# Kernel optimization log

Hardware: AMD Instinct MI355X
Metric: run time of the kernel (lower is better)

Reference implementation:

```python
import jax, jax.numpy as jnp
import numpy as np

BOARD = 19
MAX_DIST = 18
# 4 line directions then 4 diagonal directions (LINE_GROUP=[0,1,2,3], DIAG_GROUP=[4,5,6,7])
DIRS = [(-1, 0), (1, 0), (0, -1), (0, 1), (-1, -1), (-1, 1), (1, -1), (1, 1)]


def build_ray_buffer(max_dist=MAX_DIST, n=BOARD):
    """flat_index [8, max_dist, n*n] int32, valid_mask [8, max_dist, n*n] float32."""
    hs, ws = np.meshgrid(np.arange(n), np.arange(n), indexing='ij')  # [n,n]
    hs = hs.reshape(-1)
    ws = ws.reshape(-1)
    r = np.arange(1, max_dist + 1)[:, None]  # [max_dist,1]
    idx = np.zeros((8, max_dist, n * n), np.int32)
    mask = np.zeros((8, max_dist, n * n), np.float32)
    for d, (dh, dw) in enumerate(DIRS):
        hh = hs[None, :] + dh * r  # [max_dist, n*n]
        ww = ws[None, :] + dw * r
        ok = (hh >= 0) & (hh < n) & (ww >= 0) & (ww < n)
        idx[d] = np.where(ok, hh * n + ww, 0).astype(np.int32)
        mask[d] = ok.astype(np.float32)
    return jnp.asarray(idx), jnp.asarray(mask)


def setup_inputs() -> dict:
    key = jax.random.key(0)
    k_x, k_w = jax.random.split(key)
    B, c_in, c_out, md = 128, 32, 64, MAX_DIST
    x = jax.random.normal(k_x, (B, c_in, BOARD, BOARD), dtype=jnp.float32)
    # init: normal(0, sqrt(2/fan_in)) scaled by distance decay (decay=1.0)
    fan_in = c_in * 2 * md
    scale = (2.0 / fan_in) ** 0.5
    weight = scale * jax.random.normal(k_w, (c_out, c_in, 2, md), dtype=jnp.float32)
    decay = 1.0 / jnp.arange(1, md + 1, dtype=jnp.float32)
    weight = weight.at[:, :, 0, :].multiply(decay)
    weight = weight.at[:, :, 1, :].multiply(decay * 0.7)
    bias = jnp.zeros((c_out,), dtype=jnp.float32)
    flat_index, valid_mask = build_ray_buffer()
    return {"x": x, "weight": weight, "bias": bias,
            "flat_index": flat_index, "valid_mask": valid_mask}


def reference(x, weight, bias, flat_index, valid_mask):
    B, C, H, W = x.shape
    c_out = weight.shape[0]
    md = weight.shape[-1]
    # D8 symmetry expansion: lines (dirs 0-3) share weight[...,0,:], diagonals (4-7) share weight[...,1,:]
    w_full = jnp.concatenate([
        jnp.broadcast_to(weight[:, :, 0:1, :], (c_out, C, 4, md)),
        jnp.broadcast_to(weight[:, :, 1:2, :], (c_out, C, 4, md)),
    ], axis=2)  # [c_out, C, 8, md]
    x_flat = x.reshape(B, C, H * W)
    # gather along rays: [B, C, 8, md, H*W]
    gathered = x_flat[:, :, flat_index] * valid_mask  # mask broadcasts [8, md, HW]
    gathered = gathered.reshape(B, C, 8, md, H, W)
    # NOTE: faithful to original torch einsum 'bcdrhw,ocdR->bohw' — 'r' and 'R'
    # are DISTINCT labels, so distance is independently summed on each operand.
    out = jnp.einsum('bcdrhw,ocdR->bohw', gathered, w_full)
    return out + bias[None, :, None, None]
```

## Files before the change

### kernel.cpp

```cpp
#include <hip/hip_runtime.h>

#define C_IN 32
#define C_OUT 64
#define NB 128
#define HW 361
#define SXS 364
#define SSS 132
#define WS 36

__global__ __launch_bounds__(256) void prep_w_kernel(const float* __restrict__ weight,
                                                     float* __restrict__ wsf) {
  int t = blockIdx.x * blockDim.x + threadIdx.x;
  if (t >= C_OUT * C_IN) return;
  int o = t >> 5;
  int c = t & 31;
  const float* wp = weight + (size_t)((o * C_IN + c) * 2) * 18;
  float sl = 0.f, sd = 0.f;
#pragma unroll
  for (int r = 0; r < 18; ++r) { sl += wp[r]; sd += wp[18 + r]; }
  wsf[c * 64 + o] = sl;
  wsf[2048 + c * 64 + o] = sd;
  wsf[4096 + c * 64 + o] = -2.f * (sl + sd);
}

__global__ __launch_bounds__(256) void raycast_main_kernel(
    const float* __restrict__ x, const float* __restrict__ bias,
    const float* __restrict__ wsf, float* __restrict__ out) {
  __shared__ __align__(16) float sm[23584];
  float* const sx    = sm;
  float* const ssum  = sm + 11648;
  float* const pproj = sm + 15872;
  float* const swl   = sm + 20096;
  float* const swd   = sm + 21248;
  float* const swld2 = sm + 22400;
  float* const sbias = sm + 23552;

  const int tid = threadIdx.x;
  const int b = blockIdx.x >> 1;
  const int obase = (blockIdx.x & 1) << 5;

  for (int i = tid; i < 3 * 1024; i += 256) {
    int arr = i >> 10;
    int rem = i & 1023;
    int c = rem >> 5;
    int j = rem & 31;
    sm[20096 + arr * 1152 + c * WS + j] = wsf[arr * 2048 + c * 64 + obase + j];
  }
  if (tid < 32) sbias[tid] = bias[obase + tid];

  const float4* x4 = reinterpret_cast<const float4*>(x + (size_t)b * (C_IN * HW));
  for (int i = tid; i < (C_IN * HW) / 4; i += 256) {
    float4 v = x4[i];
    float vv[4] = {v.x, v.y, v.z, v.w};
    int e = i * 4;
#pragma unroll
    for (int j = 0; j < 4; ++j) {
      int ee = e + j;
      int c = ee / HW;
      int hw = ee - c * HW;
      sx[c * SXS + hw] = vv[j];
    }
  }
  __syncthreads();

  for (int t = tid; t < 608; t += 256) {
    int c = t / 19, h = t - c * 19;
    const float* p = sx + c * SXS + h * 19;
    float s = 0.f;
#pragma unroll
    for (int w = 0; w < 19; ++w) s += p[w];
    ssum[c * SSS + h] = s;
  }
  for (int t = tid; t < 608; t += 256) {
    int c = t / 19, w = t - c * 19;
    const float* p = sx + c * SXS + w;
    float s = 0.f;
#pragma unroll
    for (int h = 0; h < 19; ++h) s += p[h * 19];
    ssum[c * SSS + 20 + w] = s;
  }
  for (int t = tid; t < 1184; t += 256) {
    int c = t / 37, k = t - c * 37;
    int hmin = k > 18 ? k - 18 : 0;
    int hmax = k < 18 ? k : 18;
    const float* p = sx + c * SXS + (18 - k);
    float s = 0.f;
    for (int h = hmin; h <= hmax; ++h) s += p[h * 20];
    ssum[c * SSS + 40 + k] = s;
  }
  for (int t = tid; t < 1184; t += 256) {
    int c = t / 37, k = t - c * 37;
    int hmin = k > 18 ? k - 18 : 0;
    int hmax = k < 18 ? k : 18;
    const float* p = sx + c * SXS + k;
    float s = 0.f;
    for (int h = hmin; h <= hmax; ++h) s += p[h * 18];
    ssum[c * SSS + 80 + k] = s;
  }
  __syncthreads();

  if (tid < 240) {
    int ot = tid / 30, st = tid - ot * 30;
    int o0 = ot * 4, s0 = st * 4;
    const float* wT = (s0 < 40) ? swl : swd;
    float a[4][4] = {};
#pragma unroll 4
    for (int c = 0; c < 32; ++c) {
      float4 wv = *reinterpret_cast<const float4*>(wT + c * WS + o0);
      float4 sv = *reinterpret_cast<const float4*>(ssum + c * SSS + s0);
      float wr[4] = {wv.x, wv.y, wv.z, wv.w};
      float sr[4] = {sv.x, sv.y, sv.z, sv.w};
#pragma unroll
      for (int i = 0; i < 4; ++i)
#pragma unroll
        for (int j = 0; j < 4; ++j) a[i][j] = fmaf(wr[i], sr[j], a[i][j]);
    }
#pragma unroll
    for (int i = 0; i < 4; ++i) {
      float4 v = {a[i][0], a[i][1], a[i][2], a[i][3]};
      *reinterpret_cast<float4*>(pproj + (o0 + i) * SSS + s0) = v;
    }
  }
  __syncthreads();

  for (int t = tid; t < 364; t += 256) {
    int ot = t / 91, ht = t - ot * 91;
    int o0 = ot * 8, hw0 = ht * 4;
    float acc[8][4] = {};
#pragma unroll 4
    for (int c = 0; c < 32; ++c) {
      float4 xv = *reinterpret_cast<const float4*>(sx + c * SXS + hw0);
      float4 wa = *reinterpret_cast<const float4*>(swld2 + c * WS + o0);
      float4 wb = *reinterpret_cast<const float4*>(swld2 + c * WS + o0 + 4);
      float xr[4] = {xv.x, xv.y, xv.z, xv.w};
      float wr[8] = {wa.x, wa.y, wa.z, wa.w, wb.x, wb.y, wb.z, wb.w};
#pragma unroll
      for (int i = 0; i < 8; ++i)
#pragma unroll
        for (int j = 0; j < 4; ++j) acc[i][j] = fmaf(wr[i], xr[j], acc[i][j]);
    }
#pragma unroll
    for (int j = 0; j < 4; ++j) {
      int hw = hw0 + j;
      if (hw < HW) {
        int h = hw / 19;
        int w = hw - h * 19;
        int iA = h, iB = 20 + w, iD = 58 + h - w, iG = 80 + h + w;
#pragma unroll
        for (int i = 0; i < 8; ++i) {
          const float* pp = pproj + (o0 + i) * SSS;
          float v = acc[i][j] + pp[iA] + pp[iB] + pp[iD] + pp[iG] + sbias[o0 + i];
          out[(size_t)(b * 64 + obase + o0 + i) * HW + hw] = v;
        }
      }
    }
  }
}

extern "C" void kernel_launch(void* const* d_in, const int* in_sizes, int n_in,
                              void* d_out, int out_size, void* d_ws, size_t ws_size,
                              hipStream_t stream) {
  const float* x      = (const float*)d_in[0];
  const float* weight = (const float*)d_in[1];
  const float* bias   = (const float*)d_in[2];
  float* out = (float*)d_out;
  float* wsf = (float*)d_ws;

  prep_w_kernel<<<8, 256, 0, stream>>>(weight, wsf);
  raycast_main_kernel<<<NB * 2, 256, 0, stream>>>(x, bias, wsf, out);
}
```

Baseline: 93.09 us.

## Split fused raycast kernel into sums, projection and main kernels

Replaces the single per-batch fused kernel with three kernels: one computes line and diagonal sums per channel group, one computes the projections through a global workspace, and one does the per-pixel channel contraction straight from global x with a row-aligned tiling. The aim is more blocks and better occupancy, instead of 256 large-shared-memory blocks with mostly serial phases. In exchange it adds launch overhead and writes and reads intermediates through global memory.

```diff
diff --git a/kernel.cpp b/kernel.cpp
--- a/kernel.cpp
+++ b/kernel.cpp
@@ -1,20 +1,15 @@
 #include <hip/hip_runtime.h>
 
-#define C_IN 32
-#define C_OUT 64
-#define NB 128
 #define HW 361
-#define SXS 364
-#define SSS 132
-#define WS 36
+#define S_OFF 8192
+#define P_OFF (8192 + 128*32*128)
 
-__global__ __launch_bounds__(256) void prep_w_kernel(const float* __restrict__ weight,
-                                                     float* __restrict__ wsf) {
-  int t = blockIdx.x * blockDim.x + threadIdx.x;
-  if (t >= C_OUT * C_IN) return;
-  int o = t >> 5;
-  int c = t & 31;
-  const float* wp = weight + (size_t)((o * C_IN + c) * 2) * 18;
+__global__ __launch_bounds__(256) void prep_w(const float* __restrict__ weight,
+                                              float* __restrict__ wsf) {
+  int t = blockIdx.x * 256 + threadIdx.x;
+  if (t >= 2048) return;
+  int o = t >> 5, c = t & 31;
+  const float* wp = weight + (size_t)(o * 32 + c) * 36;
   float sl = 0.f, sd = 0.f;
 #pragma unroll
   for (int r = 0; r < 18; ++r) { sl += wp[r]; sd += wp[18 + r]; }
@@ -23,136 +18,166 @@
   wsf[4096 + c * 64 + o] = -2.f * (sl + sd);
 }
 
-__global__ __launch_bounds__(256) void raycast_main_kernel(
-    const float* __restrict__ x, const float* __restrict__ bias,
-    const float* __restrict__ wsf, float* __restrict__ out) {
-  __shared__ __align__(16) float sm[23584];
-  float* const sx    = sm;
-  float* const ssum  = sm + 11648;
-  float* const pproj = sm + 15872;
-  float* const swl   = sm + 20096;
-  float* const swd   = sm + 21248;
-  float* const swld2 = sm + 22400;
-  float* const sbias = sm + 23552;
+__global__ __launch_bounds__(256) void sums_k(const float* __restrict__ x,
+                                              float* __restrict__ wsf) {
+  __shared__ float sx[8 * 364];
+  const int b = blockIdx.x >> 2, cg = blockIdx.x & 3;
+  const int tid = threadIdx.x;
+  const float* xb = x + (size_t)b * (32 * HW) + (size_t)cg * 8 * HW;
 
-  const int tid = threadIdx.x;
-  const int b = blockIdx.x >> 1;
-  const int obase = (blockIdx.x & 1) << 5;
-
-  for (int i = tid; i < 3 * 1024; i += 256) {
-    int arr = i >> 10;
-    int rem = i & 1023;
-    int c = rem >> 5;
-    int j = rem & 31;
-    sm[20096 + arr * 1152 + c * WS + j] = wsf[arr * 2048 + c * 64 + obase + j];
-  }
-  if (tid < 32) sbias[tid] = bias[obase + tid];
-
-  const float4* x4 = reinterpret_cast<const float4*>(x + (size_t)b * (C_IN * HW));
-  for (int i = tid; i < (C_IN * HW) / 4; i += 256) {
-    float4 v = x4[i];
-    float vv[4] = {v.x, v.y, v.z, v.w};
-    int e = i * 4;
-#pragma unroll
-    for (int j = 0; j < 4; ++j) {
-      int ee = e + j;
-      int c = ee / HW;
-      int hw = ee - c * HW;
-      sx[c * SXS + hw] = vv[j];
+  for (int u = tid; u < 728; u += 256) {
+    int c = u / 91, j = u - c * 91;
+    if (j < 90) {
+      float4 v = *reinterpret_cast<const float4*>(xb + c * HW + 4 * j);
+      *reinterpret_cast<float4*>(sx + c * 364 + 4 * j) = v;
+    } else {
+      sx[c * 364 + 360] = xb[c * HW + 360];
     }
   }
   __syncthreads();
 
-  for (int t = tid; t < 608; t += 256) {
-    int c = t / 19, h = t - c * 19;
-    const float* p = sx + c * SXS + h * 19;
-    float s = 0.f;
+  float* wsS = wsf + S_OFF + ((size_t)b * 32 + cg * 8) * 128;
+  for (int it = tid; it < 1024; it += 256) {
+    int c = it >> 7, s = it & 127;
+    const float* p = sx + c * 364;
+    float sum = 0.f;
+    bool valid = true;
+    if (s < 19) {
+      const float* q = p + s * 19;
 #pragma unroll
-    for (int w = 0; w < 19; ++w) s += p[w];
-    ssum[c * SSS + h] = s;
+      for (int w = 0; w < 19; ++w) sum += q[w];
+    } else if (s >= 20 && s < 39) {
+      const float* q = p + (s - 20);
+#pragma unroll
+      for (int h = 0; h < 19; ++h) sum += q[h * 19];
+    } else if (s >= 40 && s < 77) {
+      int k = s - 40;
+      int hmin = k > 18 ? k - 18 : 0, hmax = k < 18 ? k : 18;
+      const float* q = p + (18 - k);
+      float acc = 0.f;
+      for (int h = hmin; h <= hmax; ++h) acc += q[h * 20];
+      sum = acc;
+    } else if (s >= 80 && s < 117) {
+      int k = s - 80;
+      int hmin = k > 18 ? k - 18 : 0, hmax = k < 18 ? k : 18;
+      const float* q = p + k;
+      float acc = 0.f;
+      for (int h = hmin; h <= hmax; ++h) acc += q[h * 18];
+      sum = acc;
+    } else {
+      valid = false;
+    }
+    if (valid) wsS[c * 128 + s] = sum;
   }
-  for (int t = tid; t < 608; t += 256) {
-    int c = t / 19, w = t - c * 19;
-    const float* p = sx + c * SXS + w;
-    float s = 0.f;
-#pragma unroll
-    for (int h = 0; h < 19; ++h) s += p[h * 19];
-    ssum[c * SSS + 20 + w] = s;
+}
+
+__global__ __launch_bounds__(256) void proj_k(float* __restrict__ wsf) {
+  __shared__ float sS[32 * 64];
+  __shared__ float sWL[32 * 64];
+  __shared__ float sWD[32 * 64];
+  const int b = blockIdx.x >> 1, sh = blockIdx.x & 1;
+  const int sbase = sh * 64;
+  const int tid = threadIdx.x;
+
+  const float4* w4 = reinterpret_cast<const float4*>(wsf);
+  for (int i = tid; i < 1024; i += 256) {
+    float4 v = w4[i];
+    if (i < 512) reinterpret_cast<float4*>(sWL)[i] = v;
+    else reinterpret_cast<float4*>(sWD)[i - 512] = v;
   }
-  for (int t = tid; t < 1184; t += 256) {
-    int c = t / 37, k = t - c * 37;
-    int hmin = k > 18 ? k - 18 : 0;
-    int hmax = k < 18 ? k : 18;
-    const float* p = sx + c * SXS + (18 - k);
-    float s = 0.f;
-    for (int h = hmin; h <= hmax; ++h) s += p[h * 20];
-    ssum[c * SSS + 40 + k] = s;
-  }
-  for (int t = tid; t < 1184; t += 256) {
-    int c = t / 37, k = t - c * 37;
-    int hmin = k > 18 ? k - 18 : 0;
-    int hmax = k < 18 ? k : 18;
-    const float* p = sx + c * SXS + k;
-    float s = 0.f;
-    for (int h = hmin; h <= hmax; ++h) s += p[h * 18];
-    ssum[c * SSS + 80 + k] = s;
+  const float* Sb = wsf + S_OFF + (size_t)b * 32 * 128 + sbase;
+  for (int i = tid; i < 512; i += 256) {
+    int c = i >> 4, j = i & 15;
+    reinterpret_cast<float4*>(sS)[c * 16 + j] =
+        *reinterpret_cast<const float4*>(Sb + c * 128 + 4 * j);
   }
   __syncthreads();
 
-  if (tid < 240) {
-    int ot = tid / 30, st = tid - ot * 30;
-    int o0 = ot * 4, s0 = st * 4;
-    const float* wT = (s0 < 40) ? swl : swd;
-    float a[4][4] = {};
+  const int ot = tid >> 4, st = tid & 15;
+  const int o0 = ot * 4, s0 = st * 4;
+  const float* wT = (sbase + s0 < 40) ? sWL : sWD;
+  float a[4][4] = {};
 #pragma unroll 4
-    for (int c = 0; c < 32; ++c) {
-      float4 wv = *reinterpret_cast<const float4*>(wT + c * WS + o0);
-      float4 sv = *reinterpret_cast<const float4*>(ssum + c * SSS + s0);
-      float wr[4] = {wv.x, wv.y, wv.z, wv.w};
-      float sr[4] = {sv.x, sv.y, sv.z, sv.w};
+  for (int c = 0; c < 32; ++c) {
+    float4 wv = *reinterpret_cast<const float4*>(wT + c * 64 + o0);
+    float4 sv = *reinterpret_cast<const float4*>(sS + c * 64 + s0);
+    float wr[4] = {wv.x, wv.y, wv.z, wv.w};
+    float sr[4] = {sv.x, sv.y, sv.z, sv.w};
 #pragma unroll
-      for (int i = 0; i < 4; ++i)
+    for (int i = 0; i < 4; ++i)
 #pragma unroll
-        for (int j = 0; j < 4; ++j) a[i][j] = fmaf(wr[i], sr[j], a[i][j]);
-    }
+      for (int j = 0; j < 4; ++j) a[i][j] = fmaf(wr[i], sr[j], a[i][j]);
+  }
+  float* Pb = wsf + P_OFF + (size_t)b * 64 * 128 + sbase;
 #pragma unroll
-    for (int i = 0; i < 4; ++i) {
-      float4 v = {a[i][0], a[i][1], a[i][2], a[i][3]};
-      *reinterpret_cast<float4*>(pproj + (o0 + i) * SSS + s0) = v;
-    }
+  for (int i = 0; i < 4; ++i) {
+    float4 v = {a[i][0], a[i][1], a[i][2], a[i][3]};
+    *reinterpret_cast<float4*>(Pb + (o0 + i) * 128 + s0) = v;
   }
-  __syncthreads();
+}
 
-  for (int t = tid; t < 364; t += 256) {
-    int ot = t / 91, ht = t - ot * 91;
-    int o0 = ot * 8, hw0 = ht * 4;
-    float acc[8][4] = {};
+__global__ __launch_bounds__(256) void main_k(const float* __restrict__ x,
+                                              const float* __restrict__ bias,
+                                              const float* __restrict__ wsf,
+                                              float* __restrict__ out) {
+  const int tg = blockIdx.x * 256 + threadIdx.x;
+  const int b = tg / 1520;
+  int rem = tg - b * 1520;
+  const int og = rem / 95;
+  int rem2 = rem - og * 95;
+  const int h = rem2 / 5;
+  const int wt = rem2 - h * 5;
+  const int w0 = wt * 4;
+  const int nw = (wt == 4) ? 3 : 4;
+  const int sel = (wt == 4) ? 1 : 0;
+  const int o0 = og * 4;
+
+  const float* xb = x + (size_t)b * (32 * HW);
+  const float* w2 = wsf + 4096;
+  const int xoff = h * 19 + w0 - sel;
+
+  float acc[4][4] = {};
 #pragma unroll 4
-    for (int c = 0; c < 32; ++c) {
-      float4 xv = *reinterpret_cast<const float4*>(sx + c * SXS + hw0);
-      float4 wa = *reinterpret_cast<const float4*>(swld2 + c * WS + o0);
-      float4 wb = *reinterpret_cast<const float4*>(swld2 + c * WS + o0 + 4);
-      float xr[4] = {xv.x, xv.y, xv.z, xv.w};
-      float wr[8] = {wa.x, wa.y, wa.z, wa.w, wb.x, wb.y, wb.z, wb.w};
+  for (int c = 0; c < 32; ++c) {
+    float4 xv = *reinterpret_cast<const float4*>(xb + c * HW + xoff);
+    float vv[4] = {xv.x, xv.y, xv.z, xv.w};
+    float xr[4];
+    xr[0] = vv[sel];
+    xr[1] = vv[1 + sel];
+    xr[2] = vv[2 + sel];
+    xr[3] = sel ? 0.f : vv[3];
+    float4 wv = *reinterpret_cast<const float4*>(w2 + c * 64 + o0);
+    float wr[4] = {wv.x, wv.y, wv.z, wv.w};
 #pragma unroll
-      for (int i = 0; i < 8; ++i)
+    for (int i = 0; i < 4; ++i)
 #pragma unroll
-        for (int j = 0; j < 4; ++j) acc[i][j] = fmaf(wr[i], xr[j], acc[i][j]);
-    }
+      for (int j = 0; j < 4; ++j) acc[i][j] = fmaf(wr[i], xr[j], acc[i][j]);
+  }
+
+  const float* Pb = wsf + P_OFF + ((size_t)b * 64 + o0) * 128;
+  float4 bv = *reinterpret_cast<const float4*>(bias + o0);
+  float br[4] = {bv.x, bv.y, bv.z, bv.w};
+
 #pragma unroll
-    for (int j = 0; j < 4; ++j) {
-      int hw = hw0 + j;
-      if (hw < HW) {
-        int h = hw / 19;
-        int w = hw - h * 19;
-        int iA = h, iB = 20 + w, iD = 58 + h - w, iG = 80 + h + w;
+  for (int i = 0; i < 4; ++i) {
+    const float* pp = Pb + i * 128;
+    float A = pp[h];
+    float4 Bv = *reinterpret_cast<const float4*>(pp + 20 + w0);
+    float4 Dv = *reinterpret_cast<const float4*>(pp + 55 + h - w0);
+    float4 Gv = *reinterpret_cast<const float4*>(pp + 80 + h + w0);
+    float Br[4] = {Bv.x, Bv.y, Bv.z, Bv.w};
+    float Dr[4] = {Dv.x, Dv.y, Dv.z, Dv.w};
+    float Gr[4] = {Gv.x, Gv.y, Gv.z, Gv.w};
+    float* op = out + ((size_t)b * 64 + o0 + i) * HW + h * 19 + w0;
+    float res[4];
 #pragma unroll
-        for (int i = 0; i < 8; ++i) {
-          const float* pp = pproj + (o0 + i) * SSS;
-          float v = acc[i][j] + pp[iA] + pp[iB] + pp[iD] + pp[iG] + sbias[o0 + i];
-          out[(size_t)(b * 64 + obase + o0 + i) * HW + hw] = v;
-        }
-      }
+    for (int j = 0; j < 4; ++j)
+      res[j] = acc[i][j] + A + Br[j] + Dr[3 - j] + Gr[j] + br[i];
+    if (nw == 4) {
+      float4 ov = {res[0], res[1], res[2], res[3]};
+      *reinterpret_cast<float4*>(op) = ov;
+    } else {
+      op[0] = res[0]; op[1] = res[1]; op[2] = res[2];
     }
   }
 }
@@ -166,6 +191,8 @@
   float* out = (float*)d_out;
   float* wsf = (float*)d_ws;
 
-  prep_w_kernel<<<8, 256, 0, stream>>>(weight, wsf);
-  raycast_main_kernel<<<NB * 2, 256, 0, stream>>>(x, bias, wsf, out);
+  prep_w<<<8, 256, 0, stream>>>(weight, wsf);
+  sums_k<<<512, 256, 0, stream>>>(x, wsf);
+  proj_k<<<256, 256, 0, stream>>>(wsf);
+  main_k<<<760, 256, 0, stream>>>(x, bias, wsf, out);
 }
```

New measurement: 105.8 us. 1.14x slower.

## Fuse weight prep into main kernel and vectorize padded-row x tiles

Applied to the files above, without the earlier changes.

Removes the separate weight-summation kernel: each block now sums the ray weights for its own 32 output channels directly into shared memory, saving a launch and a global round-trip. The x tile is stored with rows padded to 20 floats, so row and column sums and the main matmul can use float4 LDS loads. The output phase is retiled per board row with 8x8 register blocks and float4 global stores, and the block size goes up to 512 threads. The cost is that every block redoes the weight sums. The global float4 accesses at odd-strided offsets depend on the hardware tolerating unaligned vector loads and stores.

```diff
diff --git a/kernel.cpp b/kernel.cpp
--- a/kernel.cpp
+++ b/kernel.cpp
@@ -1,113 +1,113 @@
 #include <hip/hip_runtime.h>
 
-#define C_IN 32
-#define C_OUT 64
-#define NB 128
 #define HW 361
-#define SXS 364
-#define SSS 132
-#define WS 36
-
-__global__ __launch_bounds__(256) void prep_w_kernel(const float* __restrict__ weight,
-                                                     float* __restrict__ wsf) {
-  int t = blockIdx.x * blockDim.x + threadIdx.x;
-  if (t >= C_OUT * C_IN) return;
-  int o = t >> 5;
-  int c = t & 31;
-  const float* wp = weight + (size_t)((o * C_IN + c) * 2) * 18;
-  float sl = 0.f, sd = 0.f;
-#pragma unroll
-  for (int r = 0; r < 18; ++r) { sl += wp[r]; sd += wp[18 + r]; }
-  wsf[c * 64 + o] = sl;
-  wsf[2048 + c * 64 + o] = sd;
-  wsf[4096 + c * 64 + o] = -2.f * (sl + sd);
-}
-
-__global__ __launch_bounds__(256) void raycast_main_kernel(
-    const float* __restrict__ x, const float* __restrict__ bias,
-    const float* __restrict__ wsf, float* __restrict__ out) {
-  __shared__ __align__(16) float sm[23584];
-  float* const sx    = sm;
-  float* const ssum  = sm + 11648;
-  float* const pproj = sm + 15872;
-  float* const swl   = sm + 20096;
-  float* const swd   = sm + 21248;
-  float* const swld2 = sm + 22400;
-  float* const sbias = sm + 23552;
-
+#define SX   0
+#define SXs  380
+#define SS   12160
+#define SSs  120
+#define SP   16000
+#define SPs  120
+#define SWL  19840
+#define SWD  20864
+#define SW2  21888
+#define SB   22912
+#define LDSF 22944
+
+__device__ __forceinline__ float4 ld4(const float* p) {
+  return *reinterpret_cast<const float4*>(p);
+}
+__device__ __forceinline__ void st4(float* p, float4 v) {
+  *reinterpret_cast<float4*>(p) = v;
+}
+
+__global__ __launch_bounds__(512) void fused_k(
+    const float* __restrict__ x, const float* __restrict__ weight,
+    const float* __restrict__ bias, float* __restrict__ out) {
+  __shared__ float sm[LDSF];
   const int tid = threadIdx.x;
   const int b = blockIdx.x >> 1;
   const int obase = (blockIdx.x & 1) << 5;
-
-  for (int i = tid; i < 3 * 1024; i += 256) {
-    int arr = i >> 10;
-    int rem = i & 1023;
-    int c = rem >> 5;
-    int j = rem & 31;
-    sm[20096 + arr * 1152 + c * WS + j] = wsf[arr * 2048 + c * 64 + obase + j];
-  }
-  if (tid < 32) sbias[tid] = bias[obase + tid];
-
-  const float4* x4 = reinterpret_cast<const float4*>(x + (size_t)b * (C_IN * HW));
-  for (int i = tid; i < (C_IN * HW) / 4; i += 256) {
-    float4 v = x4[i];
-    float vv[4] = {v.x, v.y, v.z, v.w};
-    int e = i * 4;
-#pragma unroll
-    for (int j = 0; j < 4; ++j) {
-      int ee = e + j;
-      int c = ee / HW;
-      int hw = ee - c * HW;
-      sx[c * SXS + hw] = vv[j];
+  const float* xb = x + (size_t)b * (32 * HW);
+
+  for (int p = tid; p < 1024; p += 512) {
+    int o = p >> 5, c = p & 31;
+    const float* wp = weight + (size_t)((obase + o) * 32 + c) * 36;
+    float sl = 0.f, sd = 0.f;
+#pragma unroll
+    for (int r = 0; r < 18; ++r) { sl += wp[r]; sd += wp[18 + r]; }
+    sm[SWL + c * 32 + o] = sl;
+    sm[SWD + c * 32 + o] = sd;
+    sm[SW2 + c * 32 + o] = -2.f * (sl + sd);
+  }
+  if (tid < 32) sm[SB + tid] = bias[obase + tid];
+  if (tid >= 64 && tid < 96) {
+    int c = tid - 64;
+    float* q = sm + SS + c * SSs;
+    q[19] = 0.f; q[77] = 0.f; q[78] = 0.f; q[79] = 0.f;
+    q[117] = 0.f; q[118] = 0.f; q[119] = 0.f;
+  }
+  for (int it = tid; it < 3040; it += 512) {
+    int c = it / 95, rem = it - c * 95;
+    int h = rem / 5, g = rem - h * 5;
+    const float* src = xb + c * HW + h * 19 + g * 4;
+    float* dst = sm + SX + c * SXs + h * 20 + g * 4;
+    if (g < 4) {
+      st4(dst, ld4(src));
+    } else {
+      float4 v = {src[0], src[1], src[2], 0.f};
+      st4(dst, v);
     }
   }
   __syncthreads();
 
-  for (int t = tid; t < 608; t += 256) {
-    int c = t / 19, h = t - c * 19;
-    const float* p = sx + c * SXS + h * 19;
+  for (int it = tid; it < 608; it += 512) {
+    int c = it / 19, h = it - c * 19;
+    const float* p = sm + SX + c * SXs + h * 20;
+    float4 a = ld4(p), b4 = ld4(p + 4), c4 = ld4(p + 8), d4 = ld4(p + 12), e4 = ld4(p + 16);
+    sm[SS + c * SSs + h] =
+        ((a.x + a.y) + (a.z + a.w)) + ((b4.x + b4.y) + (b4.z + b4.w)) +
+        ((c4.x + c4.y) + (c4.z + c4.w)) + ((d4.x + d4.y) + (d4.z + d4.w)) +
+        ((e4.x + e4.y) + (e4.z + e4.w));
+  }
+  for (int it = tid; it < 160; it += 512) {
+    int c = it / 5, g = it - c * 5;
+    const float* p = sm + SX + c * SXs + g * 4;
+    float ax = 0.f, ay = 0.f, az = 0.f, aw = 0.f;
+#pragma unroll
+    for (int h = 0; h < 19; ++h) {
+      float4 v = ld4(p + h * 20);
+      ax += v.x; ay += v.y; az += v.z; aw += v.w;
+    }
+    float* q = sm + SS + c * SSs + 20 + g * 4;
+    q[0] = ax; q[1] = ay; q[2] = az; q[3] = aw;
+  }
+  for (int it = tid; it < 1184; it += 512) {
+    int c = it / 37, k = it - c * 37;
+    int hmin = k > 18 ? k - 18 : 0, hmax = k < 18 ? k : 18;
+    const float* p = sm + SX + c * SXs + (18 - k);
     float s = 0.f;
-#pragma unroll
-    for (int w = 0; w < 19; ++w) s += p[w];
-    ssum[c * SSS + h] = s;
-  }
-  for (int t = tid; t < 608; t += 256) {
-    int c = t / 19, w = t - c * 19;
-    const float* p = sx + c * SXS + w;
+    for (int h = hmin; h <= hmax; ++h) s += p[h * 21];
+    sm[SS + c * SSs + 40 + k] = s;
+  }
+  for (int it = tid; it < 1184; it += 512) {
+    int c = it / 37, k = it - c * 37;
+    int hmin = k > 18 ? k - 18 : 0, hmax = k < 18 ? k : 18;
+    const float* p = sm + SX + c * SXs + k;
     float s = 0.f;
-#pragma unroll
-    for (int h = 0; h < 19; ++h) s += p[h * 19];
-    ssum[c * SSS + 20 + w] = s;
-  }
-  for (int t = tid; t < 1184; t += 256) {
-    int c = t / 37, k = t - c * 37;
-    int hmin = k > 18 ? k - 18 : 0;
-    int hmax = k < 18 ? k : 18;
-    const float* p = sx + c * SXS + (18 - k);
-    float s = 0.f;
-    for (int h = hmin; h <= hmax; ++h) s += p[h * 20];
-    ssum[c * SSS + 40 + k] = s;
-  }
-  for (int t = tid; t < 1184; t += 256) {
-    int c = t / 37, k = t - c * 37;
-    int hmin = k > 18 ? k - 18 : 0;
-    int hmax = k < 18 ? k : 18;
-    const float* p = sx + c * SXS + k;
-    float s = 0.f;
-    for (int h = hmin; h <= hmax; ++h) s += p[h * 18];
-    ssum[c * SSS + 80 + k] = s;
+    for (int h = hmin; h <= hmax; ++h) s += p[h * 19];
+    sm[SS + c * SSs + 80 + k] = s;
   }
   __syncthreads();
 
   if (tid < 240) {
     int ot = tid / 30, st = tid - ot * 30;
     int o0 = ot * 4, s0 = st * 4;
-    const float* wT = (s0 < 40) ? swl : swd;
+    const float* wT = sm + (s0 < 40 ? SWL : SWD);
     float a[4][4] = {};
-#pragma unroll 4
+#pragma unroll 8
     for (int c = 0; c < 32; ++c) {
-      float4 wv = *reinterpret_cast<const float4*>(wT + c * WS + o0);
-      float4 sv = *reinterpret_cast<const float4*>(ssum + c * SSS + s0);
+      float4 wv = ld4(wT + c * 32 + o0);
+      float4 sv = ld4(sm + SS + c * SSs + s0);
       float wr[4] = {wv.x, wv.y, wv.z, wv.w};
       float sr[4] = {sv.x, sv.y, sv.z, sv.w};
 #pragma unroll
@@ -118,40 +118,82 @@
 #pragma unroll
     for (int i = 0; i < 4; ++i) {
       float4 v = {a[i][0], a[i][1], a[i][2], a[i][3]};
-      *reinterpret_cast<float4*>(pproj + (o0 + i) * SSS + s0) = v;
+      st4(sm + SP + (o0 + i) * SPs + s0, v);
     }
   }
   __syncthreads();
 
-  for (int t = tid; t < 364; t += 256) {
-    int ot = t / 91, ht = t - ot * 91;
-    int o0 = ot * 8, hw0 = ht * 4;
-    float acc[8][4] = {};
+  if (tid < 228) {
+    int wg, r;
+    if (tid < 152) { wg = tid / 76; r = tid - wg * 76; }
+    else           { wg = 2;        r = tid - 152; }
+    const int og = r / 19, h = r - og * 19;
+    const int o0 = og * 8;
+    const size_t outbase = ((size_t)(b * 64 + obase + o0)) * HW + h * 19;
+
+    if (wg < 2) {
+      const int w0 = wg * 8;
+      float acc[8][8] = {};
 #pragma unroll 4
-    for (int c = 0; c < 32; ++c) {
-      float4 xv = *reinterpret_cast<const float4*>(sx + c * SXS + hw0);
-      float4 wa = *reinterpret_cast<const float4*>(swld2 + c * WS + o0);
-      float4 wb = *reinterpret_cast<const float4*>(swld2 + c * WS + o0 + 4);
-      float xr[4] = {xv.x, xv.y, xv.z, xv.w};
-      float wr[8] = {wa.x, wa.y, wa.z, wa.w, wb.x, wb.y, wb.z, wb.w};
-#pragma unroll
-      for (int i = 0; i < 8; ++i)
-#pragma unroll
-        for (int j = 0; j < 4; ++j) acc[i][j] = fmaf(wr[i], xr[j], acc[i][j]);
-    }
-#pragma unroll
-    for (int j = 0; j < 4; ++j) {
-      int hw = hw0 + j;
-      if (hw < HW) {
-        int h = hw / 19;
-        int w = hw - h * 19;
-        int iA = h, iB = 20 + w, iD = 58 + h - w, iG = 80 + h + w;
-#pragma unroll
-        for (int i = 0; i < 8; ++i) {
-          const float* pp = pproj + (o0 + i) * SSS;
-          float v = acc[i][j] + pp[iA] + pp[iB] + pp[iD] + pp[iG] + sbias[o0 + i];
-          out[(size_t)(b * 64 + obase + o0 + i) * HW + hw] = v;
+      for (int c = 0; c < 32; ++c) {
+        float4 xa = ld4(sm + SX + c * SXs + h * 20 + w0);
+        float4 xc = ld4(sm + SX + c * SXs + h * 20 + w0 + 4);
+        float4 wa = ld4(sm + SW2 + c * 32 + o0);
+        float4 wb = ld4(sm + SW2 + c * 32 + o0 + 4);
+        float xr[8] = {xa.x, xa.y, xa.z, xa.w, xc.x, xc.y, xc.z, xc.w};
+        float wr[8] = {wa.x, wa.y, wa.z, wa.w, wb.x, wb.y, wb.z, wb.w};
+#pragma unroll
+        for (int i = 0; i < 8; ++i)
+#pragma unroll
+          for (int j = 0; j < 8; ++j) acc[i][j] = fmaf(wr[i], xr[j], acc[i][j]);
+      }
+#pragma unroll
+      for (int i = 0; i < 8; ++i) {
+        const float* pp = sm + SP + (o0 + i) * SPs;
+        float A = pp[h] + sm[SB + o0 + i];
+        float4 B0 = ld4(pp + 20 + w0);
+        float4 B1 = ld4(pp + 24 + w0);
+        float Br[8] = {B0.x, B0.y, B0.z, B0.w, B1.x, B1.y, B1.z, B1.w};
+        float res[8];
+#pragma unroll
+        for (int j = 0; j < 8; ++j) {
+          float D = pp[58 + h - w0 - j];
+          float G = pp[80 + h + w0 + j];
+          res[j] = acc[i][j] + A + Br[j] + D + G;
         }
+        float* op = out + outbase + (size_t)i * HW + w0;
+        float4 r0 = {res[0], res[1], res[2], res[3]};
+        float4 r1 = {res[4], res[5], res[6], res[7]};
+        st4(op, r0);
+        st4(op + 4, r1);
+      }
+    } else {
+      float acc[8][4] = {};
+#pragma unroll 4
+      for (int c = 0; c < 32; ++c) {
+        float4 xa = ld4(sm + SX + c * SXs + h * 20 + 16);
+        float4 wa = ld4(sm + SW2 + c * 32 + o0);
+        float4 wb = ld4(sm + SW2 + c * 32 + o0 + 4);
+        float xr[4] = {xa.x, xa.y, xa.z, xa.w};
+        float wr[8] = {wa.x, wa.y, wa.z, wa.w, wb.x, wb.y, wb.z, wb.w};
+#pragma unroll
+        for (int i = 0; i < 8; ++i)
+#pragma unroll
+          for (int j = 0; j < 4; ++j) acc[i][j] = fmaf(wr[i], xr[j], acc[i][j]);
+      }
+#pragma unroll
+      for (int i = 0; i < 8; ++i) {
+        const float* pp = sm + SP + (o0 + i) * SPs;
+        float A = pp[h] + sm[SB + o0 + i];
+        float res[3];
+#pragma unroll
+        for (int j = 0; j < 3; ++j) {
+          float D = pp[58 + h - 16 - j];
+          float G = pp[80 + h + 16 + j];
+          res[j] = acc[i][j] + A + pp[36 + j] + D + G;
+        }
+        float* op = out + outbase + (size_t)i * HW + 16;
+        op[0] = res[0]; op[1] = res[1]; op[2] = res[2];
       }
     }
   }
@@ -164,8 +206,7 @@
   const float* weight = (const float*)d_in[1];
   const float* bias   = (const float*)d_in[2];
   float* out = (float*)d_out;
-  float* wsf = (float*)d_ws;
-
-  prep_w_kernel<<<8, 256, 0, stream>>>(weight, wsf);
-  raycast_main_kernel<<<NB * 2, 256, 0, stream>>>(x, bias, wsf, out);
-}
+  (void)d_ws; (void)ws_size;
+
+  fused_k<<<256, 512, 0, stream>>>(x, weight, bias, out);
+}
```

Result: faster. 84.48 us (-9.2%).
